# Kernel optimization log

Measured on AMD Instinct MI355X. Metric: run time of the kernel, lower is better.

Reference implementation:

```python
import jax, jax.numpy as jnp
import numpy as np

RES = 256
RADIUS = 1.3
N_INTRS = 128
STEP = 2.0 * RADIUS / N_INTRS
GRID_DIM = 2
RANK = 8


def bilinear_sample(grid, coords):
    """grid: [C,H,W]; coords: [N,2] in [-1,1] (x->W, y->H), align_corners=True, border clamp."""
    C, H, W = grid.shape
    x = jnp.clip((coords[:, 0] + 1.0) * 0.5 * (W - 1), 0.0, W - 1)
    y = jnp.clip((coords[:, 1] + 1.0) * 0.5 * (H - 1), 0.0, H - 1)
    x0 = jnp.clip(jnp.floor(x), 0, W - 2).astype(jnp.int32)
    y0 = jnp.clip(jnp.floor(y), 0, H - 2).astype(jnp.int32)
    x1, y1 = x0 + 1, y0 + 1
    wx = x - x0
    wy = y - y0
    g00 = grid[:, y0, x0]  # [C,N]
    g01 = grid[:, y0, x1]
    g10 = grid[:, y1, x0]
    g11 = grid[:, y1, x1]
    out = (g00 * (1 - wx) * (1 - wy) + g01 * wx * (1 - wy)
           + g10 * (1 - wx) * wy + g11 * wx * wy)
    return out.T  # [N,C]


def sh_deg4(d):
    """Spherical harmonics degree 4 (16 coeffs), d: [N,3] unit dirs."""
    x, y, z = d[:, 0], d[:, 1], d[:, 2]
    xx, yy, zz = x * x, y * y, z * z
    xy, yz, xz = x * y, y * z, x * z
    return jnp.stack([
        jnp.full_like(x, 0.28209479177387814),
        -0.48860251190291987 * y,
        0.48860251190291987 * z,
        -0.48860251190291987 * x,
        1.0925484305920792 * xy,
        -1.0925484305920792 * yz,
        0.94617469575755997 * zz - 0.31539156525251999,
        -1.0925484305920792 * xz,
        0.54627421529603959 * (xx - yy),
        0.59004358992664352 * y * (-3.0 * xx + yy),
        2.8906114426405538 * xy * z,
        0.45704579946446572 * y * (1.0 - 5.0 * zz),
        0.3731763325901154 * z * (5.0 * zz - 3.0),
        0.45704579946446572 * x * (1.0 - 5.0 * zz),
        1.445305721320277 * z * (xx - yy),
        0.59004358992664352 * x * (-xx + 3.0 * yy),
    ], axis=-1)  # [N,16]


def setup_inputs() -> dict:
    key = jax.random.key(0)
    ks = jax.random.split(key, 9)
    B = 16384
    # ray origins inside the sphere so every ray hits; random unit directions
    rays_o = jax.random.normal(ks[0], (B, 3), jnp.float32) * 0.3
    rays_d = jax.random.normal(ks[1], (B, 3), jnp.float32)
    G = jax.random.normal(ks[2], (3, GRID_DIM * RANK, RES, RES), jnp.float32) * 0.1
    Fgrid = jax.random.normal(ks[3], (32, 64, 64), jnp.float32) * 0.05
    sigma_W1 = jax.random.normal(ks[4], (32, 64), jnp.float32) * (1.0 / np.sqrt(32))
    sigma_W2 = jax.random.normal(ks[5], (64, 16), jnp.float32) * (1.0 / np.sqrt(64))
    color_W1 = jax.random.normal(ks[6], (31, 64), jnp.float32) * (1.0 / np.sqrt(31))
    color_W2 = jax.random.normal(ks[7], (64, 64), jnp.float32) * (1.0 / np.sqrt(64))
    color_W3 = jax.random.normal(ks[8], (64, 3), jnp.float32) * (1.0 / np.sqrt(64))
    return {"rays_o": rays_o, "rays_d": rays_d, "G": G, "Fgrid": Fgrid,
            "sigma_W1": sigma_W1, "sigma_W2": sigma_W2,
            "color_W1": color_W1, "color_W2": color_W2, "color_W3": color_W3}


def reference(rays_o, rays_d, G, Fgrid, sigma_W1, sigma_W2, color_W1, color_W2, color_W3):
    B = rays_o.shape[0]
    d = rays_d / jnp.linalg.norm(rays_d, axis=-1, keepdims=True)
    # ray-sphere intersection (|o + t d| = RADIUS), d unit
    b = jnp.sum(rays_o * d, axis=-1)
    c = jnp.sum(rays_o * rays_o, axis=-1) - RADIUS ** 2
    disc = b * b - c
    sq = jnp.sqrt(jnp.maximum(disc, 0.0))
    near = jnp.maximum(-b - sq, 0.0)
    far = -b + sq
    ts = near[:, None] + jnp.arange(N_INTRS + 1, dtype=jnp.float32) * STEP  # [B, n+1]
    tmid = 0.5 * (ts[:, :-1] + ts[:, 1:])  # [B, n]
    mask = (disc > 0)[:, None] & (tmid <= far[:, None])  # [B, n]
    pts = rays_o[:, None, :] + d[:, None, :] * tmid[..., None]  # [B, n, 3]
    # combined rescale: ((pts/R + 1)*RES/2) * 2/RES - 1 = pts / RADIUS
    p = (pts / RADIUS).reshape(-1, 3)  # [N, 3] in ~[-1,1]
    # tri-plane sampling
    coo = jnp.stack([p[:, [0, 1]], p[:, [0, 2]], p[:, [1, 2]]])  # [3, N, 2]
    interp = jax.vmap(bilinear_sample)(G, coo)  # [3, N, GRID_DIM*RANK]
    interp = interp.reshape(3, -1, GRID_DIM, RANK)
    Gvals = interp.prod(axis=0).sum(axis=-1)  # [N, GRID_DIM]
    Fvals = bilinear_sample(Fgrid, Gvals)  # [N, feature_dim]
    h = jax.nn.relu(Fvals @ sigma_W1) @ sigma_W2  # [N, 16]
    sigma_pts = h[:, 0]
    feat = h[:, 1:]
    rd = jnp.broadcast_to(d[:, None, :], (B, N_INTRS, 3)).reshape(-1, 3)
    enc = sh_deg4(rd)  # [N, 16]
    cin = jnp.concatenate([enc, feat], axis=-1)  # [N, 31]
    col = jax.nn.relu(jax.nn.relu(cin @ color_W1) @ color_W2) @ color_W3  # [N, 3]
    mflat = mask.reshape(-1)
    sigma = jax.nn.relu(jnp.where(mflat, sigma_pts, 0.0)).reshape(B, N_INTRS)
    color = jnp.where(mflat[:, None], col, 0.0).reshape(B, N_INTRS, 3)
    # sigma2alpha + compositing (white background)
    delta = ts[:, 1:] - ts[:, :-1]
    alpha = 1.0 - jnp.exp(-sigma * delta)
    trans = jnp.cumprod(1.0 - alpha + 1e-10, axis=1)
    T = jnp.concatenate([jnp.ones_like(trans[:, :1]), trans[:, :-1]], axis=1)
    w = alpha * T  # [B, n]
    rgb = jax.nn.sigmoid(color)
    acc = jnp.sum(w, axis=1)
    out = jnp.einsum('bn,bnc->bc', w, rgb) + (1.0 - acc)[:, None]
    return out
```

## Files before the change

### kernel.cpp

```cpp
#include <hip/hip_runtime.h>
#include <math.h>

#define B_RAYS 16384
#define N_I 128
constexpr float RADIUS_ = 1.3f;
constexpr float STEP_ = 0.0203125f;

__global__ __launch_bounds__(256) void k_transposeG(const float* __restrict__ G,
                                                    float* __restrict__ Gt) {
    int pl = blockIdx.x >> 8;
    int y  = blockIdx.x & 255;
    __shared__ float tile[16][257];
    int t = threadIdx.x;
#pragma unroll
    for (int ch = 0; ch < 16; ++ch)
        tile[ch][t] = G[((pl * 16 + ch) * 256 + y) * 256 + t];
    __syncthreads();
    float* dst = Gt + (pl * 256 + y) * 256 * 16;
#pragma unroll
    for (int i = 0; i < 16; ++i) {
        int o = i * 256 + t;
        dst[o] = tile[o & 15][o >> 4];
    }
}

__global__ __launch_bounds__(256) void k_transposeF(const float* __restrict__ F,
                                                    float* __restrict__ Ft) {
    int y = blockIdx.x;
    __shared__ float tile[32][65];
    int t = threadIdx.x;
#pragma unroll
    for (int i = 0; i < 8; ++i) {
        int o = i * 256 + t;
        tile[o >> 6][o & 63] = F[((o >> 6) * 64 + y) * 64 + (o & 63)];
    }
    __syncthreads();
    float* dst = Ft + y * 64 * 32;
#pragma unroll
    for (int i = 0; i < 8; ++i) {
        int o = i * 256 + t;
        dst[o] = tile[o & 31][o >> 5];
    }
}

__global__ __launch_bounds__(256) void k_fused(
    const float* __restrict__ rays_o, const float* __restrict__ rays_d,
    const float* __restrict__ Gt, const float* __restrict__ Ft,
    const float* __restrict__ sW1, const float* __restrict__ sW2,
    const float* __restrict__ cW1, const float* __restrict__ cW2,
    const float* __restrict__ cW3, float* __restrict__ out) {
    __shared__ float w_s1t[64 * 32];
    __shared__ float w_s2[64 * 16];
    __shared__ float w_c1t[64 * 32];
    __shared__ float w_c2[64 * 64];
    __shared__ float w_c3[64 * 3];
    int tid = threadIdx.x;
    for (int i = tid; i < 2048; i += 256) { float v = sW1[i]; w_s1t[(i & 63) * 32 + (i >> 6)] = v; }
    for (int i = tid; i < 1024; i += 256) w_s2[i] = sW2[i];
    for (int i = tid; i < 1984; i += 256) { float v = cW1[i]; w_c1t[(i & 63) * 32 + (i >> 6)] = v; }
    for (int i = tid; i < 64; i += 256) w_c1t[i * 32 + 31] = 0.f;
    for (int i = tid; i < 4096; i += 256) w_c2[i] = cW2[i];
    if (tid < 192) w_c3[tid] = cW3[tid];
    __syncthreads();

    int lane = tid & 63;
    int ray  = (blockIdx.x << 2) + (tid >> 6);

    float ox = rays_o[ray * 3 + 0], oy = rays_o[ray * 3 + 1], oz = rays_o[ray * 3 + 2];
    float rx = rays_d[ray * 3 + 0], ry = rays_d[ray * 3 + 1], rz = rays_d[ray * 3 + 2];
    float nrm = sqrtf(rx * rx + ry * ry + rz * rz);
    float dx = rx / nrm, dy = ry / nrm, dz = rz / nrm;
    float bq = ox * dx + oy * dy + oz * dz;
    float cq = ox * ox + oy * oy + oz * oz - RADIUS_ * RADIUS_;
    float disc = bq * bq - cq;
    float sq = sqrtf(fmaxf(disc, 0.f));
    float tnear = fmaxf(-bq - sq, 0.f);
    float tfar = -bq + sq;

    float enc[16];
    {
        float x = dx, y = dy, z = dz;
        float xx = x * x, yy = y * y, zz = z * z;
        float xy = x * y, yz = y * z, xz = x * z;
        enc[0] = 0.28209479177387814f;
        enc[1] = -0.48860251190291987f * y;
        enc[2] = 0.48860251190291987f * z;
        enc[3] = -0.48860251190291987f * x;
        enc[4] = 1.0925484305920792f * xy;
        enc[5] = -1.0925484305920792f * yz;
        enc[6] = 0.94617469575756f * zz - 0.31539156525252f;
        enc[7] = -1.0925484305920792f * xz;
        enc[8] = 0.5462742152960396f * (xx - yy);
        enc[9] = 0.5900435899266435f * y * (-3.0f * xx + yy);
        enc[10] = 2.890611442640554f * xy * z;
        enc[11] = 0.4570457994644657f * y * (1.0f - 5.0f * zz);
        enc[12] = 0.3731763325901154f * z * (5.0f * zz - 3.0f);
        enc[13] = 0.4570457994644657f * x * (1.0f - 5.0f * zz);
        enc[14] = 1.445305721320277f * z * (xx - yy);
        enc[15] = 0.5900435899266435f * x * (-xx + 3.0f * yy);
    }

    float4 res[2];
#pragma unroll
    for (int u = 0; u < 2; ++u) {
        int s = (lane << 1) + u;
        float t0 = tnear + (float)s * STEP_;
        float t1 = tnear + (float)(s + 1) * STEP_;
        float tmid = 0.5f * (t0 + t1);
        bool mask = (disc > 0.f) && (tmid <= tfar);
        if (!mask) {
            res[u] = make_float4(0.f, 0.f, 0.f, 0.f);
        } else {
            float px = (ox + dx * tmid) / RADIUS_;
            float py = (oy + dy * tmid) / RADIUS_;
            float pz = (oz + dz * tmid) / RADIUS_;

            float prod[16];
            float cxs[3] = {px, px, py};
            float cys[3] = {py, pz, pz};
#pragma unroll
            for (int pl = 0; pl < 3; ++pl) {
                float fx = fminf(fmaxf((cxs[pl] + 1.0f) * 0.5f * 255.0f, 0.f), 255.f);
                float fy = fminf(fmaxf((cys[pl] + 1.0f) * 0.5f * 255.0f, 0.f), 255.f);
                float x0f = fminf(floorf(fx), 254.f);
                float y0f = fminf(floorf(fy), 254.f);
                int x0 = (int)x0f, y0 = (int)y0f;
                float wx = fx - x0f, wy = fy - y0f;
                float w00 = (1.f - wx) * (1.f - wy), w01 = wx * (1.f - wy);
                float w10 = (1.f - wx) * wy,        w11 = wx * wy;
                const float* b00 = Gt + ((pl * 256 + y0) * 256 + x0) * 16;
#pragma unroll
                for (int q = 0; q < 4; ++q) {
                    float4 g00 = *(const float4*)(b00 + q * 4);
                    float4 g01 = *(const float4*)(b00 + 16 + q * 4);
                    float4 g10 = *(const float4*)(b00 + 4096 + q * 4);
                    float4 g11 = *(const float4*)(b00 + 4112 + q * 4);
                    float a0 = g00.x * w00 + g01.x * w01 + g10.x * w10 + g11.x * w11;
                    float a1 = g00.y * w00 + g01.y * w01 + g10.y * w10 + g11.y * w11;
                    float a2 = g00.z * w00 + g01.z * w01 + g10.z * w10 + g11.z * w11;
                    float a3 = g00.w * w00 + g01.w * w01 + g10.w * w10 + g11.w * w11;
                    if (pl == 0) {
                        prod[q * 4 + 0] = a0; prod[q * 4 + 1] = a1;
                        prod[q * 4 + 2] = a2; prod[q * 4 + 3] = a3;
                    } else {
                        prod[q * 4 + 0] *= a0; prod[q * 4 + 1] *= a1;
                        prod[q * 4 + 2] *= a2; prod[q * 4 + 3] *= a3;
                    }
                }
            }
            float Gx = prod[0] + prod[1] + prod[2] + prod[3] + prod[4] + prod[5] + prod[6] + prod[7];
            float Gy = prod[8] + prod[9] + prod[10] + prod[11] + prod[12] + prod[13] + prod[14] + prod[15];

            float Fv[32];
            {
                float fx = fminf(fmaxf((Gx + 1.0f) * 0.5f * 63.0f, 0.f), 63.f);
                float fy = fminf(fmaxf((Gy + 1.0f) * 0.5f * 63.0f, 0.f), 63.f);
                float x0f = fminf(floorf(fx), 62.f);
                float y0f = fminf(floorf(fy), 62.f);
                int x0 = (int)x0f, y0 = (int)y0f;
                float wx = fx - x0f, wy = fy - y0f;
                float w00 = (1.f - wx) * (1.f - wy), w01 = wx * (1.f - wy);
                float w10 = (1.f - wx) * wy,        w11 = wx * wy;
                const float* f00 = Ft + (y0 * 64 + x0) * 32;
#pragma unroll
                for (int q = 0; q < 8; ++q) {
                    float4 g00 = *(const float4*)(f00 + q * 4);
                    float4 g01 = *(const float4*)(f00 + 32 + q * 4);
                    float4 g10 = *(const float4*)(f00 + 2048 + q * 4);
                    float4 g11 = *(const float4*)(f00 + 2048 + 32 + q * 4);
                    Fv[q * 4 + 0] = g00.x * w00 + g01.x * w01 + g10.x * w10 + g11.x * w11;
                    Fv[q * 4 + 1] = g00.y * w00 + g01.y * w01 + g10.y * w10 + g11.y * w11;
                    Fv[q * 4 + 2] = g00.z * w00 + g01.z * w01 + g10.z * w10 + g11.z * w11;
                    Fv[q * 4 + 3] = g00.w * w00 + g01.w * w01 + g10.w * w10 + g11.w * w11;
                }
            }

            float hh[16];
#pragma unroll
            for (int m = 0; m < 16; ++m) hh[m] = 0.f;
            for (int j = 0; j < 64; ++j) {
                const float4* wrow = (const float4*)&w_s1t[j * 32];
                float a0 = 0.f, a1 = 0.f, a2 = 0.f, a3 = 0.f;
#pragma unroll
                for (int q = 0; q < 8; ++q) {
                    float4 w = wrow[q];
                    a0 = fmaf(Fv[q * 4 + 0], w.x, a0);
                    a1 = fmaf(Fv[q * 4 + 1], w.y, a1);
                    a2 = fmaf(Fv[q * 4 + 2], w.z, a2);
                    a3 = fmaf(Fv[q * 4 + 3], w.w, a3);
                }
                float a = fmaxf((a0 + a1) + (a2 + a3), 0.f);
                const float4* w2row = (const float4*)&w_s2[j * 16];
#pragma unroll
                for (int q = 0; q < 4; ++q) {
                    float4 w = w2row[q];
                    hh[q * 4 + 0] = fmaf(a, w.x, hh[q * 4 + 0]);
                    hh[q * 4 + 1] = fmaf(a, w.y, hh[q * 4 + 1]);
                    hh[q * 4 + 2] = fmaf(a, w.z, hh[q * 4 + 2]);
                    hh[q * 4 + 3] = fmaf(a, w.w, hh[q * 4 + 3]);
                }
            }

            float c2[64];
#pragma unroll
            for (int m = 0; m < 64; ++m) c2[m] = 0.f;
            for (int j = 0; j < 64; ++j) {
                const float4* wrow = (const float4*)&w_c1t[j * 32];
                float a0 = 0.f, a1 = 0.f, a2 = 0.f, a3 = 0.f;
#pragma unroll
                for (int q = 0; q < 4; ++q) {
                    float4 w = wrow[q];
                    a0 = fmaf(enc[q * 4 + 0], w.x, a0);
                    a1 = fmaf(enc[q * 4 + 1], w.y, a1);
                    a2 = fmaf(enc[q * 4 + 2], w.z, a2);
                    a3 = fmaf(enc[q * 4 + 3], w.w, a3);
                }
#pragma unroll
                for (int q = 0; q < 4; ++q) {
                    float4 w = wrow[4 + q];
                    float e0 = hh[q * 4 + 1];
                    float e1 = hh[q * 4 + 2];
                    float e2 = hh[q * 4 + 3];
                    float e3 = (q == 3) ? 0.f : hh[q * 4 + 4];
                    a0 = fmaf(e0, w.x, a0);
                    a1 = fmaf(e1, w.y, a1);
                    a2 = fmaf(e2, w.z, a2);
                    a3 = fmaf(e3, w.w, a3);
                }
                float a = fmaxf((a0 + a1) + (a2 + a3), 0.f);
                const float4* w2row = (const float4*)&w_c2[j * 64];
#pragma unroll
                for (int q = 0; q < 16; ++q) {
                    float4 w = w2row[q];
                    c2[q * 4 + 0] = fmaf(a, w.x, c2[q * 4 + 0]);
                    c2[q * 4 + 1] = fmaf(a, w.y, c2[q * 4 + 1]);
                    c2[q * 4 + 2] = fmaf(a, w.z, c2[q * 4 + 2]);
                    c2[q * 4 + 3] = fmaf(a, w.w, c2[q * 4 + 3]);
                }
            }
            float col0 = 0.f, col1 = 0.f, col2 = 0.f;
#pragma unroll
            for (int m = 0; m < 64; ++m) {
                float v = fmaxf(c2[m], 0.f);
                col0 = fmaf(v, w_c3[m * 3 + 0], col0);
                col1 = fmaf(v, w_c3[m * 3 + 1], col1);
                col2 = fmaf(v, w_c3[m * 3 + 2], col2);
            }

            float sigma = fmaxf(hh[0], 0.f);
            float r = 1.f / (1.f + expf(-col0));
            float g = 1.f / (1.f + expf(-col1));
            float b = 1.f / (1.f + expf(-col2));
            res[u] = make_float4(sigma, r, g, b);
        }
    }

    int s0 = lane * 2;
    float4 p0 = res[0];
    float4 p1 = res[1];
    float ta = tnear + (float)s0 * STEP_;
    float tb = tnear + (float)(s0 + 1) * STEP_;
    float tc = tnear + (float)(s0 + 2) * STEP_;
    float d0 = tb - ta, d1 = tc - tb;
    float alpha0 = 1.f - expf(-p0.x * d0);
    float alpha1 = 1.f - expf(-p1.x * d1);
    float f0 = (1.f - alpha0) + 1e-10f;
    float f1 = (1.f - alpha1) + 1e-10f;
    float fp = f0 * f1;

    float P = fp;
#pragma unroll
    for (int dlt = 1; dlt < 64; dlt <<= 1) {
        float v = __shfl_up(P, dlt, 64);
        if (lane >= dlt) P *= v;
    }
    float E = __shfl_up(P, 1, 64);
    if (lane == 0) E = 1.f;

    float w0 = alpha0 * E;
    float w1 = alpha1 * (E * f0);
    float sr = w0 * p0.y + w1 * p1.y;
    float sg = w0 * p0.z + w1 * p1.z;
    float sb = w0 * p0.w + w1 * p1.w;
    float sa = w0 + w1;
#pragma unroll
    for (int m = 32; m >= 1; m >>= 1) {
        sr += __shfl_xor(sr, m, 64);
        sg += __shfl_xor(sg, m, 64);
        sb += __shfl_xor(sb, m, 64);
        sa += __shfl_xor(sa, m, 64);
    }
    if (lane == 0) {
        float bg = 1.f - sa;
        out[ray * 3 + 0] = sr + bg;
        out[ray * 3 + 1] = sg + bg;
        out[ray * 3 + 2] = sb + bg;
    }
}

extern "C" void kernel_launch(void* const* d_in, const int* in_sizes, int n_in,
                              void* d_out, int out_size, void* d_ws, size_t ws_size,
                              hipStream_t stream) {
    const float* rays_o = (const float*)d_in[0];
    const float* rays_d = (const float*)d_in[1];
    const float* G      = (const float*)d_in[2];
    const float* Fgrid  = (const float*)d_in[3];
    const float* sW1    = (const float*)d_in[4];
    const float* sW2    = (const float*)d_in[5];
    const float* cW1    = (const float*)d_in[6];
    const float* cW2    = (const float*)d_in[7];
    const float* cW3    = (const float*)d_in[8];
    float* out = (float*)d_out;

    char* ws = (char*)d_ws;
    float* Gt = (float*)ws;
    float* Ft = (float*)(ws + 12582912);

    k_transposeG<<<768, 256, 0, stream>>>(G, Gt);
    k_transposeF<<<64, 256, 0, stream>>>(Fgrid, Ft);
    k_fused<<<B_RAYS / 4, 256, 0, stream>>>(
        rays_o, rays_d, Gt, Ft, sW1, sW2, cW1, cW2, cW3, out);
}
```

Baseline: 870.5 us.

## Move MLP weights from LDS to global/scalar loads and set occupancy hint

Removes the per-block shared-memory staging of all MLP weights and the block-wide barrier. The weight transposes move into a one-time prep kernel, and the fused kernel reads weights directly from global memory. Because every lane uses the same addresses, those reads can become uniform scalar loads through the constant cache. The launch bounds now request 4 blocks per CU, and the freed LDS allows higher occupancy. The risk is that uniform global loads may not become scalar loads and could instead compete with the grid gathers, and the occupancy hint may cause register spills, given the 64-float accumulator.

```diff
diff --git a/kernel.cpp b/kernel.cpp
--- a/kernel.cpp
+++ b/kernel.cpp
@@ -43,26 +43,28 @@
     }
 }
 
-__global__ __launch_bounds__(256) void k_fused(
+__global__ __launch_bounds__(256) void k_prepW(const float* __restrict__ sW1,
+                                               const float* __restrict__ cW1,
+                                               float* __restrict__ w_s1t,
+                                               float* __restrict__ w_c1t) {
+    int t = threadIdx.x;
+    for (int i = t; i < 2048; i += 256) {
+        int j = i & 63, k = i >> 6;
+        w_s1t[j * 32 + k] = sW1[i];
+    }
+    for (int i = t; i < 2048; i += 256) {
+        int j = i & 63, k = i >> 6;
+        w_c1t[j * 32 + k] = (k < 31) ? cW1[k * 64 + j] : 0.f;
+    }
+}
+
+__global__ __launch_bounds__(256, 4) void k_fused(
     const float* __restrict__ rays_o, const float* __restrict__ rays_d,
     const float* __restrict__ Gt, const float* __restrict__ Ft,
-    const float* __restrict__ sW1, const float* __restrict__ sW2,
-    const float* __restrict__ cW1, const float* __restrict__ cW2,
+    const float* __restrict__ w_s1t, const float* __restrict__ sW2,
+    const float* __restrict__ w_c1t, const float* __restrict__ cW2,
     const float* __restrict__ cW3, float* __restrict__ out) {
-    __shared__ float w_s1t[64 * 32];
-    __shared__ float w_s2[64 * 16];
-    __shared__ float w_c1t[64 * 32];
-    __shared__ float w_c2[64 * 64];
-    __shared__ float w_c3[64 * 3];
-    int tid = threadIdx.x;
-    for (int i = tid; i < 2048; i += 256) { float v = sW1[i]; w_s1t[(i & 63) * 32 + (i >> 6)] = v; }
-    for (int i = tid; i < 1024; i += 256) w_s2[i] = sW2[i];
-    for (int i = tid; i < 1984; i += 256) { float v = cW1[i]; w_c1t[(i & 63) * 32 + (i >> 6)] = v; }
-    for (int i = tid; i < 64; i += 256) w_c1t[i * 32 + 31] = 0.f;
-    for (int i = tid; i < 4096; i += 256) w_c2[i] = cW2[i];
-    if (tid < 192) w_c3[tid] = cW3[tid];
-    __syncthreads();
-
+    int tid  = threadIdx.x;
     int lane = tid & 63;
     int ray  = (blockIdx.x << 2) + (tid >> 6);
 
@@ -179,7 +181,7 @@
 #pragma unroll
             for (int m = 0; m < 16; ++m) hh[m] = 0.f;
             for (int j = 0; j < 64; ++j) {
-                const float4* wrow = (const float4*)&w_s1t[j * 32];
+                const float4* wrow = (const float4*)(w_s1t + j * 32);
                 float a0 = 0.f, a1 = 0.f, a2 = 0.f, a3 = 0.f;
 #pragma unroll
                 for (int q = 0; q < 8; ++q) {
@@ -190,7 +192,7 @@
                     a3 = fmaf(Fv[q * 4 + 3], w.w, a3);
                 }
                 float a = fmaxf((a0 + a1) + (a2 + a3), 0.f);
-                const float4* w2row = (const float4*)&w_s2[j * 16];
+                const float4* w2row = (const float4*)(sW2 + j * 16);
 #pragma unroll
                 for (int q = 0; q < 4; ++q) {
                     float4 w = w2row[q];
@@ -205,7 +207,7 @@
 #pragma unroll
             for (int m = 0; m < 64; ++m) c2[m] = 0.f;
             for (int j = 0; j < 64; ++j) {
-                const float4* wrow = (const float4*)&w_c1t[j * 32];
+                const float4* wrow = (const float4*)(w_c1t + j * 32);
                 float a0 = 0.f, a1 = 0.f, a2 = 0.f, a3 = 0.f;
 #pragma unroll
                 for (int q = 0; q < 4; ++q) {
@@ -228,7 +230,7 @@
                     a3 = fmaf(e3, w.w, a3);
                 }
                 float a = fmaxf((a0 + a1) + (a2 + a3), 0.f);
-                const float4* w2row = (const float4*)&w_c2[j * 64];
+                const float4* w2row = (const float4*)(cW2 + j * 64);
 #pragma unroll
                 for (int q = 0; q < 16; ++q) {
                     float4 w = w2row[q];
@@ -242,9 +244,9 @@
 #pragma unroll
             for (int m = 0; m < 64; ++m) {
                 float v = fmaxf(c2[m], 0.f);
-                col0 = fmaf(v, w_c3[m * 3 + 0], col0);
-                col1 = fmaf(v, w_c3[m * 3 + 1], col1);
-                col2 = fmaf(v, w_c3[m * 3 + 2], col2);
+                col0 = fmaf(v, cW3[m * 3 + 0], col0);
+                col1 = fmaf(v, cW3[m * 3 + 1], col1);
+                col2 = fmaf(v, cW3[m * 3 + 2], col2);
             }
 
             float sigma = fmaxf(hh[0], 0.f);
@@ -313,11 +315,14 @@
     float* out = (float*)d_out;
 
     char* ws = (char*)d_ws;
-    float* Gt = (float*)ws;
-    float* Ft = (float*)(ws + 12582912);
+    float* Gt    = (float*)ws;
+    float* Ft    = (float*)(ws + 12582912);
+    float* w_s1t = (float*)(ws + 13107200);
+    float* w_c1t = (float*)(ws + 13115392);
 
     k_transposeG<<<768, 256, 0, stream>>>(G, Gt);
     k_transposeF<<<64, 256, 0, stream>>>(Fgrid, Ft);
+    k_prepW<<<1, 256, 0, stream>>>(sW1, cW1, w_s1t, w_c1t);
     k_fused<<<B_RAYS / 4, 256, 0, stream>>>(
-        rays_o, rays_d, Gt, Ft, sW1, sW2, cW1, cW2, cW3, out);
-}
+        rays_o, rays_d, Gt, Ft, w_s1t, sW2, w_c1t, cW2, cW3, out);
+}
```

New measurement: 1.017 ms. +16.8%, slower.
